# Kernel optimization log

Measured on AMD Instinct MI355X. Metric: run time of the kernel, lower is better.

The kernel has to match this reference:

```python
import jax, jax.numpy as jnp
import numpy as np

CHANNELS = 256

def setup_inputs() -> dict:
    key = jax.random.key(0)
    ks = jax.random.split(key, 7)
    B, C, N = 4, CHANNELS, 4096
    scale = 1.0 / np.sqrt(C)
    x = jax.random.normal(ks[0], (B, C, N), dtype=jnp.float32)
    Wq = jax.random.normal(ks[1], (C, C), dtype=jnp.float32) * scale
    bq = jax.random.normal(ks[2], (C,), dtype=jnp.float32) * 0.01
    Wk = jax.random.normal(ks[3], (C, C), dtype=jnp.float32) * scale
    bk = jax.random.normal(ks[4], (C,), dtype=jnp.float32) * 0.01
    Wv = jax.random.normal(ks[5], (C, C), dtype=jnp.float32) * scale
    bv = jax.random.normal(ks[6], (C,), dtype=jnp.float32) * 0.01
    return {"x": x, "Wq": Wq, "bq": bq, "Wk": Wk, "bk": bk, "Wv": Wv, "bv": bv}

def reference(x, Wq, bq, Wk, bk, Wv, bv):
    # x: [B, C, N]; 1x1 Conv1d == channel-mixing matmul
    C = x.shape[1]
    Q = jnp.einsum('oc,bcn->bon', Wq, x) + bq[None, :, None]   # [B, C, N]
    K = jnp.einsum('oc,bcn->bon', Wk, x) + bk[None, :, None]   # [B, C, N]
    V = jnp.einsum('oc,bcn->bon', Wv, x) + bv[None, :, None]   # [B, C, N]
    # attn[b, i, j] = softmax_j( Q[:, i]^T K[:, j] / sqrt(C) )
    scores = jnp.einsum('bci,bcj->bij', Q, K) / jnp.sqrt(jnp.asarray(C, x.dtype))
    attn = jax.nn.softmax(scores, axis=-1)                     # [B, N, N]
    context = jnp.einsum('bij,bcj->bci', attn, V)              # [B, C, N]
    return x + context
```

## Files before the change

### kernel.cpp

```cpp
#include <hip/hip_runtime.h>
#include <stdint.h>

#define B_ 4
#define C_ 256
#define N_ 4096
#define JS 4

typedef unsigned short u16;
typedef __attribute__((ext_vector_type(4))) float f32x4;
typedef __attribute__((ext_vector_type(16))) float f32x16;
typedef __attribute__((ext_vector_type(8))) short bf16x8;
typedef __attribute__((ext_vector_type(4))) int i32x4;

__device__ __forceinline__ u16 f2bf(float f) {
    uint32_t u = __float_as_uint(f);
    u += 0x7fffu + ((u >> 16) & 1u);
    return (u16)(u >> 16);
}
__device__ __forceinline__ float bf2f(u16 v) {
    uint32_t u = ((uint32_t)v) << 16;
    return __uint_as_float(u);
}
__device__ __forceinline__ uint32_t pkbf(float a, float b) {
    uint32_t ua = __float_as_uint(a) + 0x8000u;
    uint32_t ub = __float_as_uint(b) + 0x8000u;
    return (ua >> 16) | (ub & 0xffff0000u);
}

__device__ __forceinline__ float fexp2(float x) {
#if defined(__has_builtin)
#if __has_builtin(__builtin_amdgcn_exp2f)
    return __builtin_amdgcn_exp2f(x);
#else
    return exp2f(x);
#endif
#else
    return exp2f(x);
#endif
}

#if defined(__has_builtin)
#if __has_builtin(__builtin_amdgcn_global_load_lds)
#define HAVE_GLL 1
#endif
#endif

#ifdef HAVE_GLL
__device__ __forceinline__ void g2l16(const u16* g, u16* lbase, int lane) {
    (void)lane;
    __builtin_amdgcn_global_load_lds(
        (__attribute__((address_space(1))) void*)(uintptr_t)g,
        (__attribute__((address_space(3))) void*)lbase, 16, 0, 0);
}
#else
__device__ __forceinline__ void g2l16(const u16* g, u16* lbase, int lane) {
    *(i32x4*)(lbase + lane * 8) = *(const i32x4*)g;
}
#endif

__global__ __launch_bounds__(256) void wconv_kernel(
    const float* __restrict__ Wq, const float* __restrict__ Wk,
    const float* __restrict__ Wv, u16* __restrict__ Wb) {
    int id = blockIdx.x * 256 + threadIdx.x;
    const float* src = (id < 65536) ? Wq : ((id < 131072) ? Wk : Wv);
    int within = id & 65535;
    int mat = id >> 16;
    int o = within >> 8;
    int c = within & 255;
    int dst = ((((mat << 2) | (o >> 6)) * 2 + ((o >> 5) & 1)) * 16 + (c >> 4)) * 512
              + (((c >> 3) & 1) << 8) + ((o & 31) << 3) + (c & 7);
    Wb[dst] = f2bf(src[within]);
}

__global__ __launch_bounds__(1024, 4) void qkv_kernel(
    const float* __restrict__ x, const u16* __restrict__ Wb,
    const float* __restrict__ bq, const float* __restrict__ bk,
    const float* __restrict__ bv,
    u16* __restrict__ Qt, u16* __restrict__ Kt, u16* __restrict__ Vt) {
    const int XTS = 264;
    const int TQS = 280;
    const int TVS = 72;
    __shared__ __align__(16) u16 xT[64 * XTS];
    __shared__ __align__(16) u16 tqA[64 * TQS];
    __shared__ __align__(16) u16 tqB[64 * TQS];
    __shared__ __align__(16) u16 tv[256 * TVS];

    int blk = blockIdx.x;
    int n0  = (blk & 63) << 6;
    int b   = blk >> 6;
    int tid = threadIdx.x;
    int lane = tid & 63;
    int w = tid >> 6;
    int oct = w & 7;
    int nh = w >> 3;
    int l31 = lane & 31;
    int h = lane >> 5;

    {
        int c0 = tid >> 4;
        int nq = (tid & 15) << 2;
        const float* xb = x + ((size_t)b * C_ + c0) * N_ + n0 + nq;
        #pragma unroll
        for (int p = 0; p < 4; ++p) {
            f32x4 v = *(const f32x4*)(xb + (size_t)64 * N_ * p);
            int cc = c0 + 64 * p;
            #pragma unroll
            for (int k = 0; k < 4; ++k)
                xT[(nq + k) * XTS + cc] = f2bf(v[k]);
        }
    }
    __syncthreads();

    bf16x8 xf[16];
    #pragma unroll
    for (int ks = 0; ks < 16; ++ks)
        xf[ks] = *(const bf16x8*)(&xT[(32 * nh + l31) * XTS + 16 * ks + 8 * h]);

    #pragma unroll
    for (int mat = 0; mat < 2; ++mat) {
        const float* bias = mat ? bk : bq;
        u16* tq = mat ? tqB : tqA;
        f32x16 acc;
        #pragma unroll
        for (int r = 0; r < 16; ++r) acc[r] = 0.f;
        const u16* wA = Wb + ((size_t)(mat * 8 + oct)) * 8192 + (size_t)lane * 8;
        #pragma unroll
        for (int ks = 0; ks < 16; ++ks) {
            bf16x8 wf = *(const bf16x8*)(wA + 512 * ks);
            acc = __builtin_amdgcn_mfma_f32_32x32x16_bf16(xf[ks], wf, acc, 0, 0, 0);
        }
        int o = 32 * oct + l31;
        float bo = bias[o];
        #pragma unroll
        for (int g = 0; g < 4; ++g)
            #pragma unroll
            for (int r = 0; r < 4; ++r) {
                int n = 32 * nh + 8 * g + 4 * h + r;
                tq[n * TQS + o] = f2bf(acc[4 * g + r] + bo);
            }
    }

    {
        f32x16 acc;
        #pragma unroll
        for (int r = 0; r < 16; ++r) acc[r] = 0.f;
        const u16* wA = Wb + ((size_t)(2 * 8 + oct)) * 8192 + (size_t)lane * 8;
        #pragma unroll
        for (int ks = 0; ks < 16; ++ks) {
            bf16x8 wf = *(const bf16x8*)(wA + 512 * ks);
            acc = __builtin_amdgcn_mfma_f32_32x32x16_bf16(wf, xf[ks], acc, 0, 0, 0);
        }
        #pragma unroll
        for (int g = 0; g < 4; ++g)
            #pragma unroll
            for (int r = 0; r < 4; ++r) {
                int o = 32 * oct + 8 * g + 4 * h + r;
                tv[o * TVS + 32 * nh + l31] = f2bf(acc[4 * g + r] + bv[o]);
            }
    }
    __syncthreads();

    {
        int n = tid >> 4;
        size_t row = ((size_t)b * N_ + n0 + n) * C_;
        #pragma unroll
        for (int i2 = 0; i2 < 2; ++i2) {
            int ch = (tid & 15) + 16 * i2;
            bf16x8 vq = *(const bf16x8*)&tqA[n * TQS + ch * 8];
            *(bf16x8*)&Qt[row + ch * 8] = vq;
            int sk = ch ^ (n & 31);
            bf16x8 vk = *(const bf16x8*)&tqB[n * TQS + sk * 8];
            *(bf16x8*)&Kt[row + ch * 8] = vk;
        }
    }
    {
        int k = tid & 7;
        #pragma unroll
        for (int j = 0; j < 2; ++j) {
            int o = (tid >> 3) + 128 * j;
            bf16x8 vv = *(const bf16x8*)&tv[o * TVS + k * 8];
            int cd = k ^ (o & 7);
            *(bf16x8*)&Vt[((size_t)b * C_ + o) * N_ + n0 + cd * 8] = vv;
        }
    }
}

__device__ __forceinline__ void stage64_4w(const u16* Kb, const u16* Vb, int j0,
                                           u16* ksd, u16* vsd, int w, int lane) {
    const u16* kg = Kb + (size_t)(j0 + 16 * w) * C_ + lane * 8;
    u16* kdb = ksd + 16 * w * 256;
    #pragma unroll
    for (int rr = 0; rr < 8; ++rr)
        g2l16(kg + rr * 512, kdb + rr * 512, lane);
    const u16* vg = Vb + (size_t)(64 * w + (lane >> 3)) * N_ + j0 + (lane & 7) * 8;
    u16* vdb = vsd + 64 * w * 64;
    #pragma unroll
    for (int rr = 0; rr < 8; ++rr)
        g2l16(vg + (size_t)8 * rr * N_, vdb + rr * 512, lane);
}

__global__ __launch_bounds__(256, 2) void attn_kernel(
    const u16* __restrict__ Qt, const u16* __restrict__ Kt,
    const u16* __restrict__ Vt, u16* __restrict__ Op,
    float* __restrict__ lArr) {
    __shared__ __align__(16) u16 Ksh[64 * 256];
    __shared__ __align__(16) u16 Vsh[256 * 64];

    int blk = blockIdx.x;
    int it = blk & 31;
    int b  = (blk >> 5) & 3;
    int s  = blk >> 7;
    int i0 = it << 7;
    int tid = threadIdx.x;
    int lane = tid & 63;
    int w = tid >> 6;
    int l31 = lane & 31;
    int h = lane >> 5;

    bf16x8 qf[16];
    {
        const u16* qrow = Qt + ((size_t)b * N_ + i0 + 32 * w + l31) * C_ + 8 * h;
        #pragma unroll
        for (int ks = 0; ks < 16; ++ks) qf[ks] = *(const bf16x8*)(qrow + 16 * ks);
    }

    f32x16 oacc[8];
    #pragma unroll
    for (int mt = 0; mt < 8; ++mt)
        #pragma unroll
        for (int r = 0; r < 16; ++r) oacc[mt][r] = 0.f;
    float l_run = 0.f;

    const float sconst = 0.0625f * 1.44269504088896340736f;
    const u16* Kb = Kt + (size_t)b * N_ * C_;
    const u16* Vb = Vt + (size_t)b * C_ * N_;
    int jbase = s * (N_ / JS);
    const int NT = N_ / (64 * JS);

    stage64_4w(Kb, Vb, jbase, Ksh, Vsh, w, lane);
    __syncthreads();

    for (int jt = 0; jt < NT; ++jt) {
        const u16* ks_ = Ksh;
        const u16* vs_ = Vsh;

        f32x16 st0, st1;
        #pragma unroll
        for (int r = 0; r < 16; ++r) { st0[r] = 0.f; st1[r] = 0.f; }
        __builtin_amdgcn_s_setprio(1);
        #pragma unroll
        for (int ks = 0; ks < 16; ++ks) {
            int kc = ((2 * ks + h) ^ l31) << 3;
            bf16x8 kf0 = *(const bf16x8*)(ks_ + l31 * 256 + kc);
            bf16x8 kf1 = *(const bf16x8*)(ks_ + (32 + l31) * 256 + kc);
            st0 = __builtin_amdgcn_mfma_f32_32x32x16_bf16(kf0, qf[ks], st0, 0, 0, 0);
            st1 = __builtin_amdgcn_mfma_f32_32x32x16_bf16(kf1, qf[ks], st1, 0, 0, 0);
        }
        __builtin_amdgcn_s_setprio(0);

        float psum = 0.f;
        uint32_t pd[16];
        #pragma unroll
        for (int u = 0; u < 8; ++u) {
            const f32x16& stv = (u < 4) ? st0 : st1;
            int g = u & 3;
            #pragma unroll
            for (int d = 0; d < 2; ++d) {
                float p0 = fexp2(stv[4 * g + 2 * d + 0] * sconst);
                float p1 = fexp2(stv[4 * g + 2 * d + 1] * sconst);
                psum += p0 + p1;
                pd[u * 2 + d] = pkbf(p0, p1);
            }
        }
        psum += __shfl_xor(psum, 32);
        l_run += psum;

        bf16x8 pf[4];
        #pragma unroll
        for (int ks2 = 0; ks2 < 4; ++ks2) {
            uint32_t oA0 = pd[4 * ks2 + 0], oA1 = pd[4 * ks2 + 1];
            uint32_t oB0 = pd[4 * ks2 + 2], oB1 = pd[4 * ks2 + 3];
            uint32_t sn0 = h ? oA0 : oB0, sn1 = h ? oA1 : oB1;
            uint32_t rc0 = (uint32_t)__shfl_xor((int)sn0, 32);
            uint32_t rc1 = (uint32_t)__shfl_xor((int)sn1, 32);
            uint32_t ow0 = h ? oB0 : oA0, ow1 = h ? oB1 : oA1;
            i32x4 fr;
            fr[0] = (int)(h ? rc0 : ow0);
            fr[1] = (int)(h ? rc1 : ow1);
            fr[2] = (int)(h ? ow0 : rc0);
            fr[3] = (int)(h ? ow1 : rc1);
            pf[ks2] = *(bf16x8*)&fr;
        }

        __builtin_amdgcn_s_setprio(1);
        #pragma unroll
        for (int ks2 = 0; ks2 < 4; ++ks2) {
            int vc = ((2 * ks2 + h) ^ (l31 & 7)) << 3;
            #pragma unroll
            for (int mt = 0; mt < 8; ++mt) {
                bf16x8 vf = *(const bf16x8*)(vs_ + (32 * mt + l31) * 64 + vc);
                oacc[mt] = __builtin_amdgcn_mfma_f32_32x32x16_bf16(vf, pf[ks2], oacc[mt], 0, 0, 0);
            }
        }
        __builtin_amdgcn_s_setprio(0);

        if (jt + 1 < NT) {
            __syncthreads();
            stage64_4w(Kb, Vb, jbase + (jt + 1) * 64, Ksh, Vsh, w, lane);
            __syncthreads();
        }
    }

    int i = i0 + 32 * w + l31;
    u16* ob = Op + ((size_t)(s * B_ + b) * C_) * N_ + i;
    #pragma unroll
    for (int mt = 0; mt < 8; ++mt)
        #pragma unroll
        for (int g = 0; g < 4; ++g)
            #pragma unroll
            for (int r = 0; r < 4; ++r) {
                int c = 32 * mt + 8 * g + r + 4 * h;
                ob[(size_t)c * N_] = f2bf(oacc[mt][4 * g + r]);
            }
    if (h == 0) lArr[(size_t)(s * B_ + b) * N_ + i] = l_run;
}

__global__ __launch_bounds__(256) void merge_kernel(
    const float* __restrict__ x, const u16* __restrict__ Op,
    const float* __restrict__ lArr, float* __restrict__ out) {
    __shared__ float rLs[64];
    int blk = blockIdx.x;
    int cg = blk & 3;
    int ic = (blk >> 2) & 63;
    int b  = blk >> 8;
    int i0 = ic << 6;
    int tid = threadIdx.x;

    if (tid < 64) {
        float L = 0.f;
        #pragma unroll
        for (int s = 0; s < JS; ++s) L += lArr[(size_t)(s * B_ + b) * N_ + i0 + tid];
        rLs[tid] = 1.0f / L;
    }
    __syncthreads();

    int i8 = (tid & 7) << 3;
    int c  = (cg << 6) + ((tid >> 3) << 1);
    f32x4 rl0 = *(const f32x4*)&rLs[i8];
    f32x4 rl1 = *(const f32x4*)&rLs[i8 + 4];

    #pragma unroll
    for (int cc = 0; cc < 2; ++cc) {
        size_t xoff = ((size_t)b * C_ + c + cc) * N_ + i0 + i8;
        float acc[8];
        #pragma unroll
        for (int e = 0; e < 8; ++e) acc[e] = 0.f;
        #pragma unroll
        for (int s = 0; s < JS; ++s) {
            bf16x8 o = *(const bf16x8*)&Op[((size_t)(s * B_ + b) * C_ + c + cc) * N_ + i0 + i8];
            #pragma unroll
            for (int e = 0; e < 8; ++e) acc[e] += bf2f((u16)o[e]);
        }
        f32x4 xv0 = *(const f32x4*)&x[xoff];
        f32x4 xv1 = *(const f32x4*)&x[xoff + 4];
        f32x4 o0, o1;
        #pragma unroll
        for (int e = 0; e < 4; ++e) {
            o0[e] = fmaf(acc[e], rl0[e], xv0[e]);
            o1[e] = fmaf(acc[e + 4], rl1[e], xv1[e]);
        }
        *(f32x4*)&out[xoff] = o0;
        *(f32x4*)&out[xoff + 4] = o1;
    }
}

extern "C" void kernel_launch(void* const* d_in, const int* in_sizes, int n_in,
                              void* d_out, int out_size, void* d_ws, size_t ws_size,
                              hipStream_t stream) {
    const float* x  = (const float*)d_in[0];
    const float* Wq = (const float*)d_in[1];
    const float* bq = (const float*)d_in[2];
    const float* Wk = (const float*)d_in[3];
    const float* bk = (const float*)d_in[4];
    const float* Wv = (const float*)d_in[5];
    const float* bv = (const float*)d_in[6];
    float* out = (float*)d_out;

    u16* Wb = (u16*)d_ws;
    u16* Qt = Wb + 3 * 65536;
    u16* Kt = Qt + (size_t)B_ * N_ * C_;
    u16* Vt = Kt + (size_t)B_ * N_ * C_;
    u16* Op = Vt + (size_t)B_ * N_ * C_;
    float* lArr = (float*)(Op + (size_t)JS * B_ * C_ * N_);

    wconv_kernel<<<768, 256, 0, stream>>>(Wq, Wk, Wv, Wb);
    qkv_kernel<<<256, 1024, 0, stream>>>(x, Wb, bq, bk, bv, Qt, Kt, Vt);
    attn_kernel<<<512, 256, 0, stream>>>(Qt, Kt, Vt, Op, lArr);
    merge_kernel<<<1024, 256, 0, stream>>>(x, Op, lArr, out);
}
```

Before: 181.7 us.

## Pre-swizzle K into MFMA fragment order and read directly from global

The projection kernel now writes K in a per-64-column tile layout that matches the MFMA operand fragment order, so the attention kernel loads K fragments straight from global memory (coalesced 16-byte per lane) instead of staging them through shared memory. The freed LDS is used to double-buffer V, with the next tile's V prefetched at the start of each iteration and a single barrier per iteration. This removes K staging and one sync per tile, but every wave re-reads K from global/L2 and the MFMA loop now depends on global load latency.

```diff
diff --git a/kernel.cpp b/kernel.cpp
--- a/kernel.cpp
+++ b/kernel.cpp
@@ -166,11 +166,23 @@
         #pragma unroll
         for (int i2 = 0; i2 < 2; ++i2) {
             int ch = (tid & 15) + 16 * i2;
-            bf16x8 vq = *(const bf16x8*)&tqA[n * TQS + ch * 8];
-            *(bf16x8*)&Qt[row + ch * 8] = vq;
-            int sk = ch ^ (n & 31);
-            bf16x8 vk = *(const bf16x8*)&tqB[n * TQS + sk * 8];
-            *(bf16x8*)&Kt[row + ch * 8] = vk;
+            *(bf16x8*)&Qt[row + ch * 8] = *(const bf16x8*)&tqA[n * TQS + ch * 8];
+        }
+    }
+    {
+        #pragma unroll
+        for (int r = 0; r < 2; ++r) {
+            int u = tid + 1024 * r;
+            int lu = u & 63;
+            int ksx = (u >> 6) & 15;
+            int half = u >> 10;
+            int n = 32 * half + (lu & 31);
+            int cs = 16 * ksx + 8 * (lu >> 5);
+            bf16x8 v = *(const bf16x8*)&tqB[n * TQS + cs];
+            size_t dst = (size_t)b * ((size_t)N_ * C_)
+                       + ((size_t)((n0 >> 6) * 2 + half) * 16 + ksx) * 512
+                       + (size_t)lu * 8;
+            *(bf16x8*)&Kt[dst] = v;
         }
     }
     {
@@ -185,13 +197,8 @@
     }
 }
 
-__device__ __forceinline__ void stage64_4w(const u16* Kb, const u16* Vb, int j0,
-                                           u16* ksd, u16* vsd, int w, int lane) {
-    const u16* kg = Kb + (size_t)(j0 + 16 * w) * C_ + lane * 8;
-    u16* kdb = ksd + 16 * w * 256;
-    #pragma unroll
-    for (int rr = 0; rr < 8; ++rr)
-        g2l16(kg + rr * 512, kdb + rr * 512, lane);
+__device__ __forceinline__ void stageV_4w(const u16* Vb, int j0, u16* vsd,
+                                          int w, int lane) {
     const u16* vg = Vb + (size_t)(64 * w + (lane >> 3)) * N_ + j0 + (lane & 7) * 8;
     u16* vdb = vsd + 64 * w * 64;
     #pragma unroll
@@ -203,8 +210,7 @@
     const u16* __restrict__ Qt, const u16* __restrict__ Kt,
     const u16* __restrict__ Vt, u16* __restrict__ Op,
     float* __restrict__ lArr) {
-    __shared__ __align__(16) u16 Ksh[64 * 256];
-    __shared__ __align__(16) u16 Vsh[256 * 64];
+    __shared__ __align__(16) u16 Vsh[2 * 256 * 64];
 
     int blk = blockIdx.x;
     int it = blk & 31;
@@ -232,17 +238,24 @@
     float l_run = 0.f;
 
     const float sconst = 0.0625f * 1.44269504088896340736f;
-    const u16* Kb = Kt + (size_t)b * N_ * C_;
     const u16* Vb = Vt + (size_t)b * C_ * N_;
     int jbase = s * (N_ / JS);
     const int NT = N_ / (64 * JS);
 
-    stage64_4w(Kb, Vb, jbase, Ksh, Vsh, w, lane);
+    const u16* kfb0 = Kt + (size_t)b * ((size_t)N_ * C_)
+                    + (size_t)(jbase >> 6) * 16384 + (size_t)lane * 8;
+
+    stageV_4w(Vb, jbase, Vsh, w, lane);
     __syncthreads();
 
     for (int jt = 0; jt < NT; ++jt) {
-        const u16* ks_ = Ksh;
-        const u16* vs_ = Vsh;
+        int cur = jt & 1;
+        const u16* vs_ = Vsh + cur * 256 * 64;
+
+        if (jt + 1 < NT)
+            stageV_4w(Vb, jbase + (jt + 1) * 64, Vsh + (cur ^ 1) * 256 * 64, w, lane);
+
+        const u16* kfb = kfb0 + (size_t)jt * 16384;
 
         f32x16 st0, st1;
         #pragma unroll
@@ -250,9 +263,8 @@
         __builtin_amdgcn_s_setprio(1);
         #pragma unroll
         for (int ks = 0; ks < 16; ++ks) {
-            int kc = ((2 * ks + h) ^ l31) << 3;
-            bf16x8 kf0 = *(const bf16x8*)(ks_ + l31 * 256 + kc);
-            bf16x8 kf1 = *(const bf16x8*)(ks_ + (32 + l31) * 256 + kc);
+            bf16x8 kf0 = *(const bf16x8*)(kfb + ks * 512);
+            bf16x8 kf1 = *(const bf16x8*)(kfb + 8192 + ks * 512);
             st0 = __builtin_amdgcn_mfma_f32_32x32x16_bf16(kf0, qf[ks], st0, 0, 0, 0);
             st1 = __builtin_amdgcn_mfma_f32_32x32x16_bf16(kf1, qf[ks], st1, 0, 0, 0);
         }
@@ -303,12 +315,7 @@
             }
         }
         __builtin_amdgcn_s_setprio(0);
-
-        if (jt + 1 < NT) {
-            __syncthreads();
-            stage64_4w(Kb, Vb, jbase + (jt + 1) * 64, Ksh, Vsh, w, lane);
-            __syncthreads();
-        }
+        __syncthreads();
     }
 
     int i = i0 + 32 * w + l31;
```

Result: slower. 273.0 us (+50.3%).
